# Kernel tuning notes

Hardware: AMD Instinct MI355X
Metric: run time of the kernel (lower is better)

Reference implementation:

```python
import jax, jax.numpy as jnp
import numpy as np

B, T, H, L, NB, NL = 32, 512, 256, 2048, 256, 4
F0_MIN, F0_MAX = 0.0, 1.0
E_MIN, E_MAX = 0.0, 1.0


def setup_inputs() -> dict:
    key = jax.random.key(0)
    ks = jax.random.split(key, 12)
    s = 1.0 / np.sqrt(H)
    return {
        "x": jax.random.normal(ks[0], (B, T, H), jnp.float32),
        "src_seq": jax.random.uniform(ks[1], (B, T, 3), jnp.float32, 1.0, 8.0),
        "duration_target": jax.random.randint(ks[2], (B, T), 0, 7, jnp.int32),
        "pitch_target": jax.random.uniform(ks[3], (B, L), jnp.float32),
        "energy_target": jax.random.uniform(ks[4], (B, L), jnp.float32),
        "src_mask": jnp.zeros((B, T), bool),
        "max_len": L,
        "dur_W": jax.random.normal(ks[5], (NL, H, H), jnp.float32) * s,
        "dur_b": jnp.zeros((NL, H), jnp.float32),
        "dur_w": jax.random.normal(ks[6], (H,), jnp.float32) * s,
        "dur_b2": jnp.zeros((1,), jnp.float32),
        "pit_W": jax.random.normal(ks[7], (NL, H, H), jnp.float32) * s,
        "pit_b": jnp.zeros((NL, H), jnp.float32),
        "pit_w": jax.random.normal(ks[8], (H,), jnp.float32) * s,
        "pit_b2": jnp.zeros((1,), jnp.float32),
        "en_W": jax.random.normal(ks[9], (NL, H, H), jnp.float32) * s,
        "en_b": jnp.zeros((NL, H), jnp.float32),
        "en_w": jax.random.normal(ks[10], (H,), jnp.float32) * s,
        "en_b2": jnp.zeros((1,), jnp.float32),
        "pitch_emb": jax.random.normal(ks[11], (2 * NB, H), jnp.float32),
        "energy_emb": jax.random.normal(jax.random.fold_in(key, 99), (2 * NB, H), jnp.float32),
    }


def _predictor(h, W, b, w, b2, mask):
    # stand-in for Decoder(n_layers=4) + Linear(H, 1) head
    for i in range(NL):
        h = jax.nn.relu(jnp.einsum('blh,hk->blk', h, W[i]) + b[i])
    out = jnp.einsum('blh,h->bl', h, w) + b2[0]
    return jnp.where(mask, 0.0, out)


def _length_regulate(x, dur, max_len):
    # cumsum-based repeat_interleave: frame m maps to token searchsorted(cumsum(dur), m, 'right')
    cum = jnp.cumsum(dur, axis=1)                      # [B, T]
    mel_len = jnp.minimum(cum[:, -1], max_len)         # [B]
    frames = jnp.arange(max_len)                       # [L]
    idx = jax.vmap(lambda c: jnp.searchsorted(c, frames, side='right'))(cum)
    idx = jnp.clip(idx, 0, x.shape[1] - 1)             # [B, L]
    out = jnp.take_along_axis(x, idx[:, :, None], axis=1)  # [B, L, H]
    mel_mask = frames[None, :] >= mel_len[:, None]     # True = padding
    out = out * (~mel_mask)[:, :, None]
    return out, mel_len, mel_mask


def reference(x, src_seq, duration_target, pitch_target, energy_target, src_mask, max_len,
              dur_W, dur_b, dur_w, dur_b2, pit_W, pit_b, pit_w, pit_b2,
              en_W, en_b, en_w, en_b2, pitch_emb, energy_emb):
    # duration predictor: LengthPredictor = decoder + linear + tanh, scaled by note lengths
    d = _predictor(x, dur_W, dur_b, dur_w, dur_b2, src_mask)
    log_duration_prediction = (jnp.tanh(d) + 1.0) * src_seq[:, :, 2]

    # length regulator (training path: duration_target provided)
    xe, mel_len, mel_mask = _length_regulate(x, duration_target, max_len)

    pitch_prediction = jax.nn.relu(_predictor(xe, pit_W, pit_b, pit_w, pit_b2, mel_mask))
    p_idx = jnp.ceil((pitch_target - F0_MIN) / (F0_MAX - F0_MIN) * NB).astype(jnp.int32)
    p_emb = pitch_emb[p_idx]                            # [B, L, H]

    energy_prediction = _predictor(xe, en_W, en_b, en_w, en_b2, mel_mask)
    e_idx = jnp.ceil((energy_target - E_MIN) / (E_MAX - E_MIN) * NB).astype(jnp.int32)
    e_emb = energy_emb[e_idx]                           # [B, L, H]

    out = xe + p_emb + e_emb
    return out, log_duration_prediction, pitch_prediction, energy_prediction, mel_len, mel_mask
```

## Files before the change

kernel.cpp:

```cpp
#include <hip/hip_runtime.h>

typedef _Float16 half_t;
typedef _Float16 half4 __attribute__((ext_vector_type(4)));
typedef _Float16 half8 __attribute__((ext_vector_type(8)));
typedef float floatx4 __attribute__((ext_vector_type(4)));

#define HST 264
#define B_ 32
#define T_ 512
#define H_ 256
#define L_ 2048

__global__ __launch_bounds__(256) void setup_kernel(
    const int* __restrict__ dur,
    const float* __restrict__ pitch_t,
    const float* __restrict__ energy_t,
    const float* __restrict__ dur_W,
    const float* __restrict__ pit_W,
    const float* __restrict__ en_W,
    half_t* __restrict__ Wp,
    int* __restrict__ idx_ws,
    int* __restrict__ pi_ws,
    int* __restrict__ ei_ws,
    int* __restrict__ ml_ws,
    float* __restrict__ out4,
    float* __restrict__ out5) {
  __shared__ int cum_l[T_];
  __shared__ int ml_s;
  int bid = blockIdx.x;
  int tid = threadIdx.x;

  if (bid >= 128) {
    int g = (bid - 128) * 256 + tid;
    int lane = g & 63;
    int t = g >> 6;
    int nt = t & 15;
    int kk = (t >> 4) & 7;
    int layer = (t >> 7) & 3;
    int pred = t >> 9;
    const float* W = (pred == 0 ? dur_W : (pred == 1 ? pit_W : en_W)) + layer * 65536;
    int n = nt * 16 + (lane & 15);
    int k0 = kk * 32 + (lane >> 4) * 8;
    half8 o;
#pragma unroll
    for (int j = 0; j < 8; ++j) o[j] = (half_t)W[(k0 + j) * 256 + n];
    *(half8*)&Wp[(size_t)t * 512 + lane * 8] = o;
    return;
  }

  int b = bid >> 2;
  int chunk = bid & 3;
  if (tid < 64) {
    int l = tid;
    const int* dr = dur + b * T_;
    int v[8];
    int base = l * 8;
#pragma unroll
    for (int j = 0; j < 8; ++j) v[j] = dr[base + j];
#pragma unroll
    for (int j = 1; j < 8; ++j) v[j] += v[j - 1];
    int tot = v[7];
    int inc = tot;
    for (int d = 1; d < 64; d <<= 1) {
      int t = __shfl_up(inc, d);
      if (l >= d) inc += t;
    }
    int excl = inc - tot;
#pragma unroll
    for (int j = 0; j < 8; ++j) cum_l[base + j] = excl + v[j];
    if (l == 63) {
      int mel = min(inc, L_);
      ml_s = mel;
      if (chunk == 0) {
        ml_ws[b] = mel;
        out4[b] = (float)mel;
      }
    }
  }
  __syncthreads();
  int ml = ml_s;
#pragma unroll
  for (int j = 0; j < 2; ++j) {
    int m = chunk * 512 + j * 256 + tid;
    int lo = 0;
#pragma unroll
    for (int sh = 8; sh >= 0; --sh) {
      int c = lo + (1 << sh);
      if (c <= T_ && cum_l[c - 1] <= m) lo = c;
    }
    int idx = min(lo, T_ - 1);
    int g = b * L_ + m;
    idx_ws[g] = idx;
    pi_ws[g] = (int)ceilf(pitch_t[g] * 256.0f);
    ei_ws[g] = (int)ceilf(energy_t[g] * 256.0f);
    out5[g] = (m >= ml) ? 1.0f : 0.0f;
  }
}

#define CHUNK(WREG, BREG, NT)                                                      \
  {                                                                                \
    floatx4 a0 = {BREG.x, BREG.y, BREG.z, BREG.w};                                 \
    floatx4 a1 = a0, a2 = a0, a3 = a0;                                             \
    _Pragma("unroll")                                                              \
    for (int kk = 0; kk < 8; ++kk) {                                               \
      a0 = __builtin_amdgcn_mfma_f32_16x16x32_f16(WREG[kk], hf[0][kk], a0, 0, 0, 0); \
      a1 = __builtin_amdgcn_mfma_f32_16x16x32_f16(WREG[kk], hf[1][kk], a1, 0, 0, 0); \
      a2 = __builtin_amdgcn_mfma_f32_16x16x32_f16(WREG[kk], hf[2][kk], a2, 0, 0, 0); \
      a3 = __builtin_amdgcn_mfma_f32_16x16x32_f16(WREG[kk], hf[3][kk], a3, 0, 0, 0); \
    }                                                                              \
    int colbase = (NT) * 16 + qi * 4;                                              \
    half4 hw0, hw1, hw2, hw3;                                                      \
    hw0[0] = (half_t)fmaxf(a0[0], 0.f); hw0[1] = (half_t)fmaxf(a0[1], 0.f);        \
    hw0[2] = (half_t)fmaxf(a0[2], 0.f); hw0[3] = (half_t)fmaxf(a0[3], 0.f);        \
    hw1[0] = (half_t)fmaxf(a1[0], 0.f); hw1[1] = (half_t)fmaxf(a1[1], 0.f);        \
    hw1[2] = (half_t)fmaxf(a1[2], 0.f); hw1[3] = (half_t)fmaxf(a1[3], 0.f);        \
    hw2[0] = (half_t)fmaxf(a2[0], 0.f); hw2[1] = (half_t)fmaxf(a2[1], 0.f);        \
    hw2[2] = (half_t)fmaxf(a2[2], 0.f); hw2[3] = (half_t)fmaxf(a2[3], 0.f);        \
    hw3[0] = (half_t)fmaxf(a3[0], 0.f); hw3[1] = (half_t)fmaxf(a3[1], 0.f);        \
    hw3[2] = (half_t)fmaxf(a3[2], 0.f); hw3[3] = (half_t)fmaxf(a3[3], 0.f);        \
    *(half4*)&hlds[(0 * 16 + mi) * HST + colbase] = hw0;                           \
    *(half4*)&hlds[(1 * 16 + mi) * HST + colbase] = hw1;                           \
    *(half4*)&hlds[(2 * 16 + mi) * HST + colbase] = hw2;                           \
    *(half4*)&hlds[(3 * 16 + mi) * HST + colbase] = hw3;                           \
  }

__global__ __launch_bounds__(128, 2) void predictor_kernel(
    const float* __restrict__ x,
    const half_t* __restrict__ Wp,
    const float* __restrict__ dur_b, const float* __restrict__ dur_w, const float* __restrict__ dur_b2,
    const float* __restrict__ pit_b, const float* __restrict__ pit_w, const float* __restrict__ pit_b2,
    const float* __restrict__ en_b,  const float* __restrict__ en_w,  const float* __restrict__ en_b2,
    const int* __restrict__ idx_ws, const int* __restrict__ pi_ws, const int* __restrict__ ei_ws,
    const int* __restrict__ mlw,
    const float* __restrict__ src_seq, const unsigned char* __restrict__ src_mask,
    const float* __restrict__ pemb, const float* __restrict__ eemb,
    float* __restrict__ out0, float* __restrict__ out1,
    float* __restrict__ out2, float* __restrict__ out3) {
  __shared__ half_t hlds[64 * HST];
  int bid = blockIdx.x;
  int mode, blk;
  const half_t* W; const float* bias; const float* wh; const float* b2p; float* outp;
  if (bid < 1024)      { mode = 1; blk = bid;        W = Wp + 262144; bias = pit_b; wh = pit_w; b2p = pit_b2; outp = out2; }
  else if (bid < 2048) { mode = 2; blk = bid - 1024; W = Wp + 524288; bias = en_b;  wh = en_w;  b2p = en_b2;  outp = out3; }
  else                 { mode = 0; blk = bid - 2048; W = Wp;          bias = dur_b; wh = dur_w; b2p = dur_b2; outp = out1; }

  int tid = threadIdx.x;
  int wv = tid >> 6, lane = tid & 63;
  int mi = lane & 15, qi = lane >> 4;
  int srow0 = wv * 32;
  int brow0 = blk * 64;

  if (mode == 0) {
    for (int it = 0; it < 32; ++it) {
      int rl = srow0 + it;
      const float4 xv = *(const float4*)&x[(size_t)(brow0 + rl) * H_ + lane * 4];
      half4 h4;
      h4[0] = (half_t)xv.x; h4[1] = (half_t)xv.y;
      h4[2] = (half_t)xv.z; h4[3] = (half_t)xv.w;
      *(half4*)&hlds[rl * HST + lane * 4] = h4;
    }
  } else {
    int b = brow0 >> 11;
    int m0 = brow0 & (L_ - 1);
    int ml = mlw[b];
    for (int it = 0; it < 32; ++it) {
      int rl = srow0 + it;
      int m = m0 + rl;
      int g = b * L_ + m;
      float4 xv = {0.f, 0.f, 0.f, 0.f};
      if (m < ml) {
        int ir = idx_ws[g];
        xv = *(const float4*)&x[((size_t)(b * T_ + ir)) * H_ + lane * 4];
      }
      if (mode == 1) {
        const float4 pv = *(const float4*)&pemb[(size_t)pi_ws[g] * H_ + lane * 4];
        const float4 ev = *(const float4*)&eemb[(size_t)ei_ws[g] * H_ + lane * 4];
        floatx4 o;
        o[0] = xv.x + pv.x + ev.x;
        o[1] = xv.y + pv.y + ev.y;
        o[2] = xv.z + pv.z + ev.z;
        o[3] = xv.w + pv.w + ev.w;
        __builtin_nontemporal_store(o, (floatx4*)&out0[(size_t)g * H_ + lane * 4]);
      }
      half4 h4;
      h4[0] = (half_t)xv.x; h4[1] = (half_t)xv.y;
      h4[2] = (half_t)xv.z; h4[3] = (half_t)xv.w;
      *(half4*)&hlds[rl * HST + lane * 4] = h4;
    }
  }
  __syncthreads();

  int nt0 = wv * 8;
  half8 wA[8], wB[8];
  float4 bA, bB;
#pragma unroll
  for (int kk = 0; kk < 8; ++kk)
    wA[kk] = *(const half8*)&W[(size_t)(kk * 16 + nt0) * 512 + lane * 8];
  bA = *(const float4*)&bias[nt0 * 16 + qi * 4];

#pragma unroll 1
  for (int layer = 0; layer < 4; ++layer) {
    const half_t* wl = W + (size_t)layer * 65536;
    const float* bl = bias + layer * 256;

    half8 hf[4][8];
#pragma unroll
    for (int mt = 0; mt < 4; ++mt)
#pragma unroll
      for (int kk = 0; kk < 8; ++kk)
        hf[mt][kk] = *(const half8*)&hlds[(mt * 16 + mi) * HST + kk * 32 + qi * 8];
    __syncthreads();

#pragma unroll
    for (int ntp = 0; ntp < 4; ++ntp) {
      int ntA = nt0 + ntp * 2;
#pragma unroll
      for (int kk = 0; kk < 8; ++kk)
        wB[kk] = *(const half8*)&wl[(size_t)(kk * 16 + ntA + 1) * 512 + lane * 8];
      bB = *(const float4*)&bl[(ntA + 1) * 16 + qi * 4];
      CHUNK(wA, bA, ntA);
      if (ntp < 3) {
#pragma unroll
        for (int kk = 0; kk < 8; ++kk)
          wA[kk] = *(const half8*)&wl[(size_t)(kk * 16 + ntA + 2) * 512 + lane * 8];
        bA = *(const float4*)&bl[(ntA + 2) * 16 + qi * 4];
      } else if (layer < 3) {
#pragma unroll
        for (int kk = 0; kk < 8; ++kk)
          wA[kk] = *(const half8*)&wl[(size_t)(65536 + (kk * 16 + nt0) * 512) + lane * 8];
        bA = *(const float4*)&bl[256 + nt0 * 16 + qi * 4];
      }
      CHUNK(wB, bB, ntA + 1);
    }
    __syncthreads();
  }

  {
    int r = lane >> 1, hf2 = lane & 1;
    int rl = srow0 + r;
    float sum = 0.f;
    const half_t* hrow = &hlds[rl * HST + hf2 * 128];
    const float* whp = wh + hf2 * 128;
#pragma unroll
    for (int j = 0; j < 16; ++j) {
      half8 hv = *(const half8*)&hrow[j * 8];
#pragma unroll
      for (int u = 0; u < 8; ++u) sum += (float)hv[u] * whp[j * 8 + u];
    }
    sum += __shfl_xor(sum, 1);
    if (hf2 == 0) {
      int row = brow0 + rl;
      float d = sum + b2p[0];
      if (mode == 0) {
        if (src_mask[row]) d = 0.f;
        float s2 = src_seq[(size_t)row * 3 + 2];
        outp[row] = (tanhf(d) + 1.0f) * s2;
      } else {
        int b = row >> 11;
        int m = row & (L_ - 1);
        float v = (m >= mlw[b]) ? 0.f : d;
        outp[row] = (mode == 1) ? fmaxf(v, 0.f) : v;
      }
    }
  }
}

extern "C" void kernel_launch(void* const* d_in, const int* in_sizes, int n_in,
                              void* d_out, int out_size, void* d_ws, size_t ws_size,
                              hipStream_t stream) {
  const float* x        = (const float*)d_in[0];
  const float* src_seq  = (const float*)d_in[1];
  const int*   durt     = (const int*)d_in[2];
  const float* pitcht   = (const float*)d_in[3];
  const float* energyt  = (const float*)d_in[4];
  const unsigned char* src_mask = (const unsigned char*)d_in[5];
  const float* dur_W  = (const float*)d_in[7];
  const float* dur_b  = (const float*)d_in[8];
  const float* dur_w  = (const float*)d_in[9];
  const float* dur_b2 = (const float*)d_in[10];
  const float* pit_W  = (const float*)d_in[11];
  const float* pit_b  = (const float*)d_in[12];
  const float* pit_w  = (const float*)d_in[13];
  const float* pit_b2 = (const float*)d_in[14];
  const float* en_W   = (const float*)d_in[15];
  const float* en_b   = (const float*)d_in[16];
  const float* en_w   = (const float*)d_in[17];
  const float* en_b2  = (const float*)d_in[18];
  const float* pemb   = (const float*)d_in[19];
  const float* eemb   = (const float*)d_in[20];

  float* out0 = (float*)d_out;
  float* out1 = out0 + 16777216;
  float* out2 = out1 + 16384;
  float* out3 = out2 + 65536;
  float* out4 = out3 + 65536;
  float* out5 = out4 + 32;

  int* idx_ws = (int*)d_ws;
  int* pi_ws  = idx_ws + 65536;
  int* ei_ws  = pi_ws + 65536;
  int* ml_ws  = ei_ws + 65536;
  half_t* Wp  = (half_t*)((char*)d_ws + 786560);

  setup_kernel<<<dim3(512), dim3(256), 0, stream>>>(
      durt, pitcht, energyt, dur_W, pit_W, en_W, Wp,
      idx_ws, pi_ws, ei_ws, ml_ws, out4, out5);
  predictor_kernel<<<dim3(2304), dim3(128), 0, stream>>>(
      x, Wp,
      dur_b, dur_w, dur_b2,
      pit_b, pit_w, pit_b2,
      en_b, en_w, en_b2,
      idx_ws, pi_ws, ei_ws, ml_ws, src_seq, src_mask, pemb, eemb,
      out0, out1, out2, out3);
}
```

Before: 268.3 us.

## Stage predictor weights in LDS with double buffering and register-resident activations

Blocks grow to 512 threads covering 256 rows. Each wave now keeps its 32 rows of activations in registers across layers, instead of the whole block sharing activations through LDS. Weights are repacked in setup and streamed into a 128KB LDS double buffer in half-layer phases, prefetched into registers during the MFMA work of the previous phase. This cuts repeated global/L2 weight reads per block and the LDS activation round-trips. The costs are a very large LDS footprint, which limits occupancy to roughly one block per CU, plus extra barriers and a small per-wave bounce buffer to transpose outputs back into the MFMA input layout.

```diff
diff --git a/kernel.cpp b/kernel.cpp
--- a/kernel.cpp
+++ b/kernel.cpp
@@ -5,7 +5,6 @@
 typedef _Float16 half8 __attribute__((ext_vector_type(8)));
 typedef float floatx4 __attribute__((ext_vector_type(4)));
 
-#define HST 264
 #define B_ 32
 #define T_ 512
 #define H_ 256
@@ -44,7 +43,8 @@
     half8 o;
 #pragma unroll
     for (int j = 0; j < 8; ++j) o[j] = (half_t)W[(k0 + j) * 256 + n];
-    *(half8*)&Wp[(size_t)t * 512 + lane * 8] = o;
+    int c = ((pred * 4 + layer) * 2 + (nt >> 3)) * 64 + kk * 8 + (nt & 7);
+    *(half8*)&Wp[(size_t)c * 512 + lane * 8] = o;
     return;
   }
 
@@ -97,34 +97,7 @@
   }
 }
 
-#define CHUNK(WREG, BREG, NT)                                                      \
-  {                                                                                \
-    floatx4 a0 = {BREG.x, BREG.y, BREG.z, BREG.w};                                 \
-    floatx4 a1 = a0, a2 = a0, a3 = a0;                                             \
-    _Pragma("unroll")                                                              \
-    for (int kk = 0; kk < 8; ++kk) {                                               \
-      a0 = __builtin_amdgcn_mfma_f32_16x16x32_f16(WREG[kk], hf[0][kk], a0, 0, 0, 0); \
-      a1 = __builtin_amdgcn_mfma_f32_16x16x32_f16(WREG[kk], hf[1][kk], a1, 0, 0, 0); \
-      a2 = __builtin_amdgcn_mfma_f32_16x16x32_f16(WREG[kk], hf[2][kk], a2, 0, 0, 0); \
-      a3 = __builtin_amdgcn_mfma_f32_16x16x32_f16(WREG[kk], hf[3][kk], a3, 0, 0, 0); \
-    }                                                                              \
-    int colbase = (NT) * 16 + qi * 4;                                              \
-    half4 hw0, hw1, hw2, hw3;                                                      \
-    hw0[0] = (half_t)fmaxf(a0[0], 0.f); hw0[1] = (half_t)fmaxf(a0[1], 0.f);        \
-    hw0[2] = (half_t)fmaxf(a0[2], 0.f); hw0[3] = (half_t)fmaxf(a0[3], 0.f);        \
-    hw1[0] = (half_t)fmaxf(a1[0], 0.f); hw1[1] = (half_t)fmaxf(a1[1], 0.f);        \
-    hw1[2] = (half_t)fmaxf(a1[2], 0.f); hw1[3] = (half_t)fmaxf(a1[3], 0.f);        \
-    hw2[0] = (half_t)fmaxf(a2[0], 0.f); hw2[1] = (half_t)fmaxf(a2[1], 0.f);        \
-    hw2[2] = (half_t)fmaxf(a2[2], 0.f); hw2[3] = (half_t)fmaxf(a2[3], 0.f);        \
-    hw3[0] = (half_t)fmaxf(a3[0], 0.f); hw3[1] = (half_t)fmaxf(a3[1], 0.f);        \
-    hw3[2] = (half_t)fmaxf(a3[2], 0.f); hw3[3] = (half_t)fmaxf(a3[3], 0.f);        \
-    *(half4*)&hlds[(0 * 16 + mi) * HST + colbase] = hw0;                           \
-    *(half4*)&hlds[(1 * 16 + mi) * HST + colbase] = hw1;                           \
-    *(half4*)&hlds[(2 * 16 + mi) * HST + colbase] = hw2;                           \
-    *(half4*)&hlds[(3 * 16 + mi) * HST + colbase] = hw3;                           \
-  }
-
-__global__ __launch_bounds__(128, 2) void predictor_kernel(
+__global__ __launch_bounds__(512, 2) void predictor_kernel(
     const float* __restrict__ x,
     const half_t* __restrict__ Wp,
     const float* __restrict__ dur_b, const float* __restrict__ dur_w, const float* __restrict__ dur_b2,
@@ -136,37 +109,39 @@
     const float* __restrict__ pemb, const float* __restrict__ eemb,
     float* __restrict__ out0, float* __restrict__ out1,
     float* __restrict__ out2, float* __restrict__ out3) {
-  __shared__ half_t hlds[64 * HST];
+  __shared__ half_t wlds[65536];
+  __shared__ half_t bounce[8][640];
+
   int bid = blockIdx.x;
-  int mode, blk;
-  const half_t* W; const float* bias; const float* wh; const float* b2p; float* outp;
-  if (bid < 1024)      { mode = 1; blk = bid;        W = Wp + 262144; bias = pit_b; wh = pit_w; b2p = pit_b2; outp = out2; }
-  else if (bid < 2048) { mode = 2; blk = bid - 1024; W = Wp + 524288; bias = en_b;  wh = en_w;  b2p = en_b2;  outp = out3; }
-  else                 { mode = 0; blk = bid - 2048; W = Wp;          bias = dur_b; wh = dur_w; b2p = dur_b2; outp = out1; }
+  int mode, blk, pred;
+  const float* bias; const float* wh; const float* b2p; float* outp;
+  if (bid < 256)      { mode = 1; blk = bid;       pred = 1; bias = pit_b; wh = pit_w; b2p = pit_b2; outp = out2; }
+  else if (bid < 512) { mode = 2; blk = bid - 256; pred = 2; bias = en_b;  wh = en_w;  b2p = en_b2;  outp = out3; }
+  else                { mode = 0; blk = bid - 512; pred = 0; bias = dur_b; wh = dur_w; b2p = dur_b2; outp = out1; }
 
   int tid = threadIdx.x;
   int wv = tid >> 6, lane = tid & 63;
   int mi = lane & 15, qi = lane >> 4;
-  int srow0 = wv * 32;
-  int brow0 = blk * 64;
-
+  int brow0 = blk * 256;
+  int wrow0 = brow0 + wv * 32;
+  const half_t* Wpp = Wp + (size_t)pred * 262144;
+
+  half_t* slice = &wlds[wv * 8192];
   if (mode == 0) {
     for (int it = 0; it < 32; ++it) {
-      int rl = srow0 + it;
-      const float4 xv = *(const float4*)&x[(size_t)(brow0 + rl) * H_ + lane * 4];
+      const float4 xv = *(const float4*)&x[(size_t)(wrow0 + it) * H_ + lane * 4];
       half4 h4;
       h4[0] = (half_t)xv.x; h4[1] = (half_t)xv.y;
       h4[2] = (half_t)xv.z; h4[3] = (half_t)xv.w;
-      *(half4*)&hlds[rl * HST + lane * 4] = h4;
+      *(half4*)&slice[it * 256 + lane * 4] = h4;
     }
   } else {
     int b = brow0 >> 11;
-    int m0 = brow0 & (L_ - 1);
     int ml = mlw[b];
+    int m0 = (brow0 & (L_ - 1)) + wv * 32;
     for (int it = 0; it < 32; ++it) {
-      int rl = srow0 + it;
-      int m = m0 + rl;
-      int g = b * L_ + m;
+      int m = m0 + it;
+      int g = wrow0 + it;
       float4 xv = {0.f, 0.f, 0.f, 0.f};
       if (m < ml) {
         int ir = idx_ws[g];
@@ -185,71 +160,113 @@
       half4 h4;
       h4[0] = (half_t)xv.x; h4[1] = (half_t)xv.y;
       h4[2] = (half_t)xv.z; h4[3] = (half_t)xv.w;
-      *(half4*)&hlds[rl * HST + lane * 4] = h4;
-    }
-  }
+      *(half4*)&slice[it * 256 + lane * 4] = h4;
+    }
+  }
+  half8 hf[2][8];
+#pragma unroll
+  for (int mt = 0; mt < 2; ++mt)
+#pragma unroll
+    for (int kk = 0; kk < 8; ++kk)
+      hf[mt][kk] = *(const half8*)&slice[(mt * 16 + mi) * 256 + kk * 32 + qi * 8];
   __syncthreads();
 
-  int nt0 = wv * 8;
-  half8 wA[8], wB[8];
-  float4 bA, bB;
-#pragma unroll
-  for (int kk = 0; kk < 8; ++kk)
-    wA[kk] = *(const half8*)&W[(size_t)(kk * 16 + nt0) * 512 + lane * 8];
-  bA = *(const float4*)&bias[nt0 * 16 + qi * 4];
+  {
+    float4 s0[8];
+#pragma unroll
+    for (int i = 0; i < 8; ++i)
+      s0[i] = *(const float4*)&Wpp[wv * 4096 + i * 512 + lane * 8];
+#pragma unroll
+    for (int i = 0; i < 8; ++i)
+      *(float4*)&wlds[wv * 4096 + i * 512 + lane * 8] = s0[i];
+  }
+  __syncthreads();
+
+  half8 hfn[2][8];
+
+#define PHASE(NH, DO_STAGE)                                                        \
+  {                                                                                \
+    const half_t* bufC = &wlds[(NH) * 32768];                                      \
+    float4 stg[8];                                                                 \
+    if (DO_STAGE) {                                                                \
+      const half_t* srcp = Wpp + (size_t)(layer * 2 + (NH) + 1) * 32768;           \
+      _Pragma("unroll")                                                            \
+      for (int i = 0; i < 8; ++i)                                                  \
+        stg[i] = *(const float4*)&srcp[wv * 4096 + i * 512 + lane * 8];            \
+    }                                                                              \
+    floatx4 acc[8][2];                                                             \
+    _Pragma("unroll")                                                              \
+    for (int u = 0; u < 8; ++u) {                                                  \
+      acc[u][0] = (floatx4){0.f, 0.f, 0.f, 0.f};                                   \
+      acc[u][1] = (floatx4){0.f, 0.f, 0.f, 0.f};                                   \
+    }                                                                              \
+    _Pragma("unroll")                                                              \
+    for (int np = 0; np < 4; ++np) {                                               \
+      _Pragma("unroll")                                                            \
+      for (int kk = 0; kk < 8; ++kk) {                                             \
+        half8 w0 = *(const half8*)&bufC[(kk * 8 + 2 * np) * 512 + lane * 8];       \
+        half8 w1 = *(const half8*)&bufC[(kk * 8 + 2 * np + 1) * 512 + lane * 8];   \
+        acc[2 * np][0]     = __builtin_amdgcn_mfma_f32_16x16x32_f16(w0, hf[0][kk], acc[2 * np][0], 0, 0, 0);     \
+        acc[2 * np][1]     = __builtin_amdgcn_mfma_f32_16x16x32_f16(w0, hf[1][kk], acc[2 * np][1], 0, 0, 0);     \
+        acc[2 * np + 1][0] = __builtin_amdgcn_mfma_f32_16x16x32_f16(w1, hf[0][kk], acc[2 * np + 1][0], 0, 0, 0); \
+        acc[2 * np + 1][1] = __builtin_amdgcn_mfma_f32_16x16x32_f16(w1, hf[1][kk], acc[2 * np + 1][1], 0, 0, 0); \
+      }                                                                            \
+    }                                                                              \
+    if (DO_STAGE) {                                                                \
+      half_t* dstp = &wlds[((NH) ^ 1) * 32768];                                    \
+      _Pragma("unroll")                                                            \
+      for (int i = 0; i < 8; ++i)                                                  \
+        *(float4*)&dstp[wv * 4096 + i * 512 + lane * 8] = stg[i];                  \
+    }                                                                              \
+    const float* bl = bias + layer * 256 + (NH) * 128;                             \
+    _Pragma("unroll")                                                              \
+    for (int mt = 0; mt < 2; ++mt) {                                               \
+      _Pragma("unroll")                                                            \
+      for (int kp = 0; kp < 4; ++kp) {                                             \
+        _Pragma("unroll")                                                          \
+        for (int hh = 0; hh < 2; ++hh) {                                           \
+          int ntl = kp * 2 + hh;                                                   \
+          float4 bv = *(const float4*)&bl[ntl * 16 + qi * 4];                      \
+          floatx4 a = acc[ntl][mt];                                                \
+          half4 h4;                                                                \
+          h4[0] = (half_t)fmaxf(a[0] + bv.x, 0.f);                                 \
+          h4[1] = (half_t)fmaxf(a[1] + bv.y, 0.f);                                 \
+          h4[2] = (half_t)fmaxf(a[2] + bv.z, 0.f);                                 \
+          h4[3] = (half_t)fmaxf(a[3] + bv.w, 0.f);                                 \
+          *(half4*)&bounce[wv][mi * 40 + hh * 16 + qi * 4] = h4;                   \
+        }                                                                          \
+        hfn[mt][(NH) * 4 + kp] = *(const half8*)&bounce[wv][mi * 40 + qi * 8];     \
+      }                                                                            \
+    }                                                                              \
+    __syncthreads();                                                               \
+  }
 
 #pragma unroll 1
   for (int layer = 0; layer < 4; ++layer) {
-    const half_t* wl = W + (size_t)layer * 65536;
-    const float* bl = bias + layer * 256;
-
-    half8 hf[4][8];
-#pragma unroll
-    for (int mt = 0; mt < 4; ++mt)
+    PHASE(0, true);
+    PHASE(1, (layer < 3));
+#pragma unroll
+    for (int mt = 0; mt < 2; ++mt)
 #pragma unroll
       for (int kk = 0; kk < 8; ++kk)
-        hf[mt][kk] = *(const half8*)&hlds[(mt * 16 + mi) * HST + kk * 32 + qi * 8];
-    __syncthreads();
-
-#pragma unroll
-    for (int ntp = 0; ntp < 4; ++ntp) {
-      int ntA = nt0 + ntp * 2;
-#pragma unroll
-      for (int kk = 0; kk < 8; ++kk)
-        wB[kk] = *(const half8*)&wl[(size_t)(kk * 16 + ntA + 1) * 512 + lane * 8];
-      bB = *(const float4*)&bl[(ntA + 1) * 16 + qi * 4];
-      CHUNK(wA, bA, ntA);
-      if (ntp < 3) {
-#pragma unroll
-        for (int kk = 0; kk < 8; ++kk)
-          wA[kk] = *(const half8*)&wl[(size_t)(kk * 16 + ntA + 2) * 512 + lane * 8];
-        bA = *(const float4*)&bl[(ntA + 2) * 16 + qi * 4];
-      } else if (layer < 3) {
-#pragma unroll
-        for (int kk = 0; kk < 8; ++kk)
-          wA[kk] = *(const half8*)&wl[(size_t)(65536 + (kk * 16 + nt0) * 512) + lane * 8];
-        bA = *(const float4*)&bl[256 + nt0 * 16 + qi * 4];
-      }
-      CHUNK(wB, bB, ntA + 1);
-    }
-    __syncthreads();
-  }
-
-  {
-    int r = lane >> 1, hf2 = lane & 1;
-    int rl = srow0 + r;
+        hf[mt][kk] = hfn[mt][kk];
+  }
+
+#pragma unroll
+  for (int mt = 0; mt < 2; ++mt) {
     float sum = 0.f;
-    const half_t* hrow = &hlds[rl * HST + hf2 * 128];
-    const float* whp = wh + hf2 * 128;
-#pragma unroll
-    for (int j = 0; j < 16; ++j) {
-      half8 hv = *(const half8*)&hrow[j * 8];
-#pragma unroll
-      for (int u = 0; u < 8; ++u) sum += (float)hv[u] * whp[j * 8 + u];
-    }
-    sum += __shfl_xor(sum, 1);
-    if (hf2 == 0) {
-      int row = brow0 + rl;
+#pragma unroll
+    for (int kk = 0; kk < 8; ++kk) {
+      float4 wa = *(const float4*)&wh[kk * 32 + qi * 8];
+      float4 wb = *(const float4*)&wh[kk * 32 + qi * 8 + 4];
+      half8 hv = hf[mt][kk];
+      sum += (float)hv[0] * wa.x + (float)hv[1] * wa.y + (float)hv[2] * wa.z + (float)hv[3] * wa.w
+           + (float)hv[4] * wb.x + (float)hv[5] * wb.y + (float)hv[6] * wb.z + (float)hv[7] * wb.w;
+    }
+    sum += __shfl_xor(sum, 16);
+    sum += __shfl_xor(sum, 32);
+    if (qi == 0) {
+      int row = wrow0 + mt * 16 + mi;
       float d = sum + b2p[0];
       if (mode == 0) {
         if (src_mask[row]) d = 0.f;
@@ -305,7 +322,7 @@
   setup_kernel<<<dim3(512), dim3(256), 0, stream>>>(
       durt, pitcht, energyt, dur_W, pit_W, en_W, Wp,
       idx_ws, pi_ws, ei_ws, ml_ws, out4, out5);
-  predictor_kernel<<<dim3(2304), dim3(128), 0, stream>>>(
+  predictor_kernel<<<dim3(576), dim3(512), 0, stream>>>(
       x, Wp,
       dur_b, dur_w, dur_b2,
       pit_b, pit_w, pit_b2,
```

Measured after the change: 315.0 us. +17.4%, slower.

## Partition predictor MLP by row per wave, removing block barriers

Applied to the files above, without the earlier changes.

Each wave now computes all 256 output columns for its own 32 rows instead of half the columns for all 64 rows. Because each wave only reads and writes its own rows in LDS, the __syncthreads between layers are removed. Weight loads use a triple-buffered rotation across 16 column tiles. The cost is that each wave now loads the full weight matrix, doubling per-block weight traffic from L2/L1, and MFMA issue per wave has fewer independent accumulators (2 instead of 4).

```diff
diff --git a/kernel.cpp b/kernel.cpp
--- a/kernel.cpp
+++ b/kernel.cpp
@@ -97,31 +97,31 @@
   }
 }
 
-#define CHUNK(WREG, BREG, NT)                                                      \
+#define LOADW(WB, BB, NT)                                                          \
   {                                                                                \
-    floatx4 a0 = {BREG.x, BREG.y, BREG.z, BREG.w};                                 \
-    floatx4 a1 = a0, a2 = a0, a3 = a0;                                             \
+    _Pragma("unroll")                                                              \
+    for (int kk = 0; kk < 8; ++kk)                                                 \
+      WB[kk] = *(const half8*)&wl[(size_t)(kk * 16 + (NT)) * 512 + lane * 8];      \
+    BB = *(const float4*)&bl[(NT) * 16 + qi * 4];                                  \
+  }
+
+#define COMP(WB, BB, NT)                                                           \
+  {                                                                                \
+    floatx4 acc0 = {BB.x, BB.y, BB.z, BB.w};                                       \
+    floatx4 acc1 = acc0;                                                           \
     _Pragma("unroll")                                                              \
     for (int kk = 0; kk < 8; ++kk) {                                               \
-      a0 = __builtin_amdgcn_mfma_f32_16x16x32_f16(WREG[kk], hf[0][kk], a0, 0, 0, 0); \
-      a1 = __builtin_amdgcn_mfma_f32_16x16x32_f16(WREG[kk], hf[1][kk], a1, 0, 0, 0); \
-      a2 = __builtin_amdgcn_mfma_f32_16x16x32_f16(WREG[kk], hf[2][kk], a2, 0, 0, 0); \
-      a3 = __builtin_amdgcn_mfma_f32_16x16x32_f16(WREG[kk], hf[3][kk], a3, 0, 0, 0); \
+      acc0 = __builtin_amdgcn_mfma_f32_16x16x32_f16(WB[kk], hf[0][kk], acc0, 0, 0, 0); \
+      acc1 = __builtin_amdgcn_mfma_f32_16x16x32_f16(WB[kk], hf[1][kk], acc1, 0, 0, 0); \
     }                                                                              \
     int colbase = (NT) * 16 + qi * 4;                                              \
-    half4 hw0, hw1, hw2, hw3;                                                      \
-    hw0[0] = (half_t)fmaxf(a0[0], 0.f); hw0[1] = (half_t)fmaxf(a0[1], 0.f);        \
-    hw0[2] = (half_t)fmaxf(a0[2], 0.f); hw0[3] = (half_t)fmaxf(a0[3], 0.f);        \
-    hw1[0] = (half_t)fmaxf(a1[0], 0.f); hw1[1] = (half_t)fmaxf(a1[1], 0.f);        \
-    hw1[2] = (half_t)fmaxf(a1[2], 0.f); hw1[3] = (half_t)fmaxf(a1[3], 0.f);        \
-    hw2[0] = (half_t)fmaxf(a2[0], 0.f); hw2[1] = (half_t)fmaxf(a2[1], 0.f);        \
-    hw2[2] = (half_t)fmaxf(a2[2], 0.f); hw2[3] = (half_t)fmaxf(a2[3], 0.f);        \
-    hw3[0] = (half_t)fmaxf(a3[0], 0.f); hw3[1] = (half_t)fmaxf(a3[1], 0.f);        \
-    hw3[2] = (half_t)fmaxf(a3[2], 0.f); hw3[3] = (half_t)fmaxf(a3[3], 0.f);        \
-    *(half4*)&hlds[(0 * 16 + mi) * HST + colbase] = hw0;                           \
-    *(half4*)&hlds[(1 * 16 + mi) * HST + colbase] = hw1;                           \
-    *(half4*)&hlds[(2 * 16 + mi) * HST + colbase] = hw2;                           \
-    *(half4*)&hlds[(3 * 16 + mi) * HST + colbase] = hw3;                           \
+    half4 h40, h41;                                                                \
+    h40[0] = (half_t)fmaxf(acc0[0], 0.f); h40[1] = (half_t)fmaxf(acc0[1], 0.f);    \
+    h40[2] = (half_t)fmaxf(acc0[2], 0.f); h40[3] = (half_t)fmaxf(acc0[3], 0.f);    \
+    h41[0] = (half_t)fmaxf(acc1[0], 0.f); h41[1] = (half_t)fmaxf(acc1[1], 0.f);    \
+    h41[2] = (half_t)fmaxf(acc1[2], 0.f); h41[3] = (half_t)fmaxf(acc1[3], 0.f);    \
+    *(half4*)&hlds[(wrow0 + mi) * HST + colbase] = h40;                            \
+    *(half4*)&hlds[(wrow0 + 16 + mi) * HST + colbase] = h41;                       \
   }
 
 __global__ __launch_bounds__(128, 2) void predictor_kernel(
@@ -147,12 +147,12 @@
   int tid = threadIdx.x;
   int wv = tid >> 6, lane = tid & 63;
   int mi = lane & 15, qi = lane >> 4;
-  int srow0 = wv * 32;
+  int wrow0 = wv * 32;
   int brow0 = blk * 64;
 
   if (mode == 0) {
     for (int it = 0; it < 32; ++it) {
-      int rl = srow0 + it;
+      int rl = wrow0 + it;
       const float4 xv = *(const float4*)&x[(size_t)(brow0 + rl) * H_ + lane * 4];
       half4 h4;
       h4[0] = (half_t)xv.x; h4[1] = (half_t)xv.y;
@@ -164,7 +164,7 @@
     int m0 = brow0 & (L_ - 1);
     int ml = mlw[b];
     for (int it = 0; it < 32; ++it) {
-      int rl = srow0 + it;
+      int rl = wrow0 + it;
       int m = m0 + rl;
       int g = b * L_ + m;
       float4 xv = {0.f, 0.f, 0.f, 0.f};
@@ -188,56 +188,46 @@
       *(half4*)&hlds[rl * HST + lane * 4] = h4;
     }
   }
-  __syncthreads();
-
-  int nt0 = wv * 8;
-  half8 wA[8], wB[8];
-  float4 bA, bB;
-#pragma unroll
-  for (int kk = 0; kk < 8; ++kk)
-    wA[kk] = *(const half8*)&W[(size_t)(kk * 16 + nt0) * 512 + lane * 8];
-  bA = *(const float4*)&bias[nt0 * 16 + qi * 4];
+
+  half8 w0[8], w1[8], w2[8];
+  float4 b0, b1, b2v;
 
 #pragma unroll 1
   for (int layer = 0; layer < 4; ++layer) {
     const half_t* wl = W + (size_t)layer * 65536;
     const float* bl = bias + layer * 256;
 
-    half8 hf[4][8];
-#pragma unroll
-    for (int mt = 0; mt < 4; ++mt)
+    LOADW(w0, b0, 0);
+    LOADW(w1, b1, 1);
+
+    half8 hf[2][8];
+#pragma unroll
+    for (int mt = 0; mt < 2; ++mt)
 #pragma unroll
       for (int kk = 0; kk < 8; ++kk)
-        hf[mt][kk] = *(const half8*)&hlds[(mt * 16 + mi) * HST + kk * 32 + qi * 8];
-    __syncthreads();
-
-#pragma unroll
-    for (int ntp = 0; ntp < 4; ++ntp) {
-      int ntA = nt0 + ntp * 2;
-#pragma unroll
-      for (int kk = 0; kk < 8; ++kk)
-        wB[kk] = *(const half8*)&wl[(size_t)(kk * 16 + ntA + 1) * 512 + lane * 8];
-      bB = *(const float4*)&bl[(ntA + 1) * 16 + qi * 4];
-      CHUNK(wA, bA, ntA);
-      if (ntp < 3) {
-#pragma unroll
-        for (int kk = 0; kk < 8; ++kk)
-          wA[kk] = *(const half8*)&wl[(size_t)(kk * 16 + ntA + 2) * 512 + lane * 8];
-        bA = *(const float4*)&bl[(ntA + 2) * 16 + qi * 4];
-      } else if (layer < 3) {
-#pragma unroll
-        for (int kk = 0; kk < 8; ++kk)
-          wA[kk] = *(const half8*)&wl[(size_t)(65536 + (kk * 16 + nt0) * 512) + lane * 8];
-        bA = *(const float4*)&bl[256 + nt0 * 16 + qi * 4];
-      }
-      CHUNK(wB, bB, ntA + 1);
-    }
-    __syncthreads();
+        hf[mt][kk] = *(const half8*)&hlds[(wrow0 + mt * 16 + mi) * HST + kk * 32 + qi * 8];
+
+    LOADW(w2, b2v, 2);  COMP(w0, b0, 0);
+    LOADW(w0, b0, 3);   COMP(w1, b1, 1);
+    LOADW(w1, b1, 4);   COMP(w2, b2v, 2);
+    LOADW(w2, b2v, 5);  COMP(w0, b0, 3);
+    LOADW(w0, b0, 6);   COMP(w1, b1, 4);
+    LOADW(w1, b1, 7);   COMP(w2, b2v, 5);
+    LOADW(w2, b2v, 8);  COMP(w0, b0, 6);
+    LOADW(w0, b0, 9);   COMP(w1, b1, 7);
+    LOADW(w1, b1, 10);  COMP(w2, b2v, 8);
+    LOADW(w2, b2v, 11); COMP(w0, b0, 9);
+    LOADW(w0, b0, 12);  COMP(w1, b1, 10);
+    LOADW(w1, b1, 13);  COMP(w2, b2v, 11);
+    LOADW(w2, b2v, 14); COMP(w0, b0, 12);
+    LOADW(w0, b0, 15);  COMP(w1, b1, 13);
+    COMP(w2, b2v, 14);
+    COMP(w0, b0, 15);
   }
 
   {
     int r = lane >> 1, hf2 = lane & 1;
-    int rl = srow0 + r;
+    int rl = wrow0 + r;
     float sum = 0.f;
     const half_t* hrow = &hlds[rl * HST + hf2 * 128];
     const float* whp = wh + hf2 * 128;
```

Measured after the change: 376.6 us. 40.4% more time.
